# Optimization experiments

Measured on AMD Instinct MI355X. Metric: run time of the kernel, lower is better.

## Reference

```python
import jax, jax.numpy as jnp
import numpy as np

N = 50000       # nodes
E = 800000      # edges (before self-loops)
IN_DIM = 128
HID = 64
HEADS = 4
C = HID // HEADS  # 16 per-head channels
NEG_SLOPE = 0.2   # PyG GATConv default
BN_EPS = 1e-5


def setup_inputs() -> dict:
    key = jax.random.key(0)
    ks = jax.random.split(key, 16)
    inp = {
        "x": jax.random.normal(ks[0], (N, IN_DIM), jnp.float32),
        "edge_index": jax.random.randint(ks[1], (2, E), 0, N, dtype=jnp.int32),
    }
    def glorot(k, shape):
        fan = sum(shape)
        return jax.random.normal(k, shape, jnp.float32) * jnp.sqrt(2.0 / fan)
    # layer 0: in=IN_DIM, layer 1: in=HID
    inp["W0"] = glorot(ks[2], (IN_DIM, HEADS * C))
    inp["a_src0"] = glorot(ks[3], (HEADS, C))
    inp["a_dst0"] = glorot(ks[4], (HEADS, C))
    inp["b0"] = jnp.zeros((HEADS * C,), jnp.float32)
    inp["g0"] = jnp.ones((HID,), jnp.float32)
    inp["be0"] = jnp.zeros((HID,), jnp.float32)
    inp["W1"] = glorot(ks[5], (HID, HEADS * C))
    inp["a_src1"] = glorot(ks[6], (HEADS, C))
    inp["a_dst1"] = glorot(ks[7], (HEADS, C))
    inp["b1"] = jnp.zeros((HEADS * C,), jnp.float32)
    inp["g1"] = jnp.ones((HID,), jnp.float32)
    inp["be1"] = jnp.zeros((HID,), jnp.float32)
    return inp


def _segment_softmax(e, dst, n):
    # softmax over edges grouped by destination node, per head. e: [Et, H]
    m = jax.ops.segment_max(e, dst, num_segments=n)          # [N, H]
    ex = jnp.exp(e - m[dst])
    s = jax.ops.segment_sum(ex, dst, num_segments=n)         # [N, H]
    return ex / (s[dst] + 1e-16)


def _gat_conv(h, src, dst, W, a_s, a_d, b):
    n = h.shape[0]
    hp = (h @ W).reshape(n, HEADS, C)                        # [N, H, C]
    al_s = jnp.einsum('nhc,hc->nh', hp, a_s)                 # [N, H]
    al_d = jnp.einsum('nhc,hc->nh', hp, a_d)
    e = jax.nn.leaky_relu(al_s[src] + al_d[dst], NEG_SLOPE)  # [Et, H]
    alpha = _segment_softmax(e, dst, n)
    msg = hp[src] * alpha[:, :, None]                        # [Et, H, C]
    out = jax.ops.segment_sum(msg, dst, num_segments=n)      # [N, H, C]
    return out.reshape(n, HEADS * C) + b


def _batch_norm(h, g, b):
    mu = h.mean(axis=0)
    var = h.var(axis=0)
    return (h - mu) * jax.lax.rsqrt(var + BN_EPS) * g + b


def reference(x, edge_index, W0, a_src0, a_dst0, b0, g0, be0,
              W1, a_src1, a_dst1, b1, g1, be1):
    n = x.shape[0]
    loops = jnp.arange(n, dtype=edge_index.dtype)
    src = jnp.concatenate([edge_index[0], loops])  # PyG adds self-loops
    dst = jnp.concatenate([edge_index[1], loops])
    h = _gat_conv(x, src, dst, W0, a_src0, a_dst0, b0)
    h = _batch_norm(h, g0, be0)
    h = jax.nn.relu(h)  # dropout: identity (eval / deterministic)
    h = _gat_conv(h, src, dst, W1, a_src1, a_dst1, b1)
    h = _batch_norm(h, g1, be1)
    return h
```

## Files before the change

kernel.cpp:

```cpp
#include <hip/hip_runtime.h>
#include <hip/hip_fp16.h>

#define CAP 128

__device__ __forceinline__ float sel4(float4 v, int h) {
  return h == 0 ? v.x : h == 1 ? v.y : h == 2 ? v.z : v.w;
}

template<int K, bool APPLY_BN>
__global__ void __launch_bounds__(256, 4)
gemm_tiled(const float* __restrict__ X, const float* __restrict__ W,
           const float* __restrict__ a_s, const float* __restrict__ a_d,
           const float* __restrict__ bnsum, const float* __restrict__ bnsq,
           const float* __restrict__ g, const float* __restrict__ be,
           __half* __restrict__ hp, float* __restrict__ al_s,
           float* __restrict__ al_d, int n)
{
  __shared__ float Wl[(K / 4) * 64 * 4];
  __shared__ float Xt[64 * K];

  for (int gi = threadIdx.x; gi < (K / 4) * 64; gi += 256) {
    int k4 = gi >> 6, ln = gi & 63;
    float4 w;
    w.x = W[(k4 * 4 + 0) * 64 + ln];
    w.y = W[(k4 * 4 + 1) * 64 + ln];
    w.z = W[(k4 * 4 + 2) * 64 + ln];
    w.w = W[(k4 * 4 + 3) * 64 + ln];
    *(float4*)&Wl[gi * 4] = w;
  }

  int row0 = blockIdx.x * 64;
  int nrows = min(64, n - row0);
  float4 sc, sh;
  if (APPLY_BN) {
    int cg = (threadIdx.x & 15) * 4;
    float inv_n = 1.f / (float)n;
#pragma unroll
    for (int q = 0; q < 4; ++q) {
      float mu  = bnsum[cg + q] * inv_n;
      float var = bnsq[cg + q] * inv_n - mu * mu;
      float s   = g[cg + q] * rsqrtf(var + 1e-5f);
      ((float*)&sc)[q] = s;
      ((float*)&sh)[q] = be[cg + q] - mu * s;
    }
  }
  const float4* src = (const float4*)(X + (size_t)row0 * K);
  int nf4 = nrows * (K / 4);
  for (int i = threadIdx.x; i < nf4; i += 256) {
    float4 v = src[i];
    if (APPLY_BN) {
      v.x = fmaxf(v.x * sc.x + sh.x, 0.f);
      v.y = fmaxf(v.y * sc.y + sh.y, 0.f);
      v.z = fmaxf(v.z * sc.z + sh.z, 0.f);
      v.w = fmaxf(v.w * sc.w + sh.w, 0.f);
    }
    *(float4*)&Xt[i * 4] = v;
  }
  __syncthreads();

  int lane = threadIdx.x & 63;
  int wid  = threadIdx.x >> 6;
  int rbase = wid * 16;
  float acc[16];
#pragma unroll
  for (int r = 0; r < 16; ++r) acc[r] = 0.f;

  for (int k4 = 0; k4 < K / 4; ++k4) {
    float4 wv = *(const float4*)&Wl[(k4 * 64 + lane) * 4];
#pragma unroll
    for (int r = 0; r < 16; ++r) {
      float4 xv = *(const float4*)&Xt[(rbase + r) * K + k4 * 4];
      acc[r] += xv.x * wv.x + xv.y * wv.y + xv.z * wv.z + xv.w * wv.w;
    }
  }

  float as_l = a_s[lane], ad_l = a_d[lane];
  int h = lane >> 4, c = lane & 15;
#pragma unroll
  for (int r = 0; r < 16; ++r) {
    int lr = rbase + r;
    if (lr >= nrows) break;
    int row = row0 + lr;
    float a = acc[r];
    hp[(size_t)row * 64 + lane] = __float2half(a);
    float vs = a * as_l;
    float vd = a * ad_l;
#pragma unroll
    for (int off = 8; off >= 1; off >>= 1) {
      vs += __shfl_xor(vs, off, 64);
      vd += __shfl_xor(vd, off, 64);
    }
    if (c == 0) { al_s[row * 4 + h] = vs; al_d[row * 4 + h] = vd; }
  }
}

__global__ void hist_k(const int* __restrict__ ei, int E, int N, int* __restrict__ count)
{
  int e = blockIdx.x * 256 + threadIdx.x;
  int Et = E + N;
  if (e >= Et) return;
  int d = (e < E) ? ei[E + e] : (e - E);
  atomicAdd(&count[d], 1);
}

__global__ void scan_block_k(const int* __restrict__ count, int* __restrict__ row_ptr,
                             int* __restrict__ partial, int n)
{
  __shared__ int woff[16];
  int tid = threadIdx.x;
  int i = blockIdx.x * 1024 + tid;
  int v = (i < n) ? count[i] : 0;
  int lane = tid & 63, wid = tid >> 6;
  int incl = v;
#pragma unroll
  for (int off = 1; off < 64; off <<= 1) {
    int t = __shfl_up(incl, off, 64);
    if (lane >= off) incl += t;
  }
  if (lane == 63) woff[wid] = incl;
  __syncthreads();
  if (tid < 16) {
    int wv = woff[tid];
    int winc = wv;
#pragma unroll
    for (int off = 1; off < 16; off <<= 1) {
      int t = __shfl_up(winc, off, 64);
      if (tid >= off) winc += t;
    }
    woff[tid] = winc - wv;
    if (tid == 15) partial[blockIdx.x] = winc;
  }
  __syncthreads();
  if (i < n) row_ptr[i] = woff[wid] + incl - v;
}

__global__ void scan_partial_k(int* __restrict__ partial, int* __restrict__ row_ptr,
                               int nb, int n)
{
  int tid = threadIdx.x;
  int v = (tid < nb) ? partial[tid] : 0;
  int incl = v;
#pragma unroll
  for (int off = 1; off < 64; off <<= 1) {
    int t = __shfl_up(incl, off, 64);
    if (tid >= off) incl += t;
  }
  if (tid < nb) partial[tid] = incl - v;
  if (tid == 63) row_ptr[n] = incl;
}

__global__ void scan_add_k(int* __restrict__ row_ptr, int* __restrict__ cursor,
                           const int* __restrict__ partial, int n)
{
  int i = blockIdx.x * 1024 + threadIdx.x;
  if (i < n) {
    int r = row_ptr[i] + partial[blockIdx.x];
    row_ptr[i] = r;
    cursor[i] = r;
  }
}

__global__ void scatter_k(const int* __restrict__ ei, int E, int N,
                          int* __restrict__ cursor, int* __restrict__ col_src,
                          int* __restrict__ col_dst)
{
  int e = blockIdx.x * 256 + threadIdx.x;
  int Et = E + N;
  if (e >= Et) return;
  int s, d;
  if (e < E) { s = ei[e]; d = ei[E + e]; } else { s = d = e - E; }
  int pos = atomicAdd(&cursor[d], 1);
  col_src[pos] = s;
  col_dst[pos] = d;
}

__global__ void eweight_k(const int* __restrict__ csrc, const int* __restrict__ cdst,
                          const float* __restrict__ al_s, const float* __restrict__ al_d,
                          float4* __restrict__ ew, int Et)
{
  int e = blockIdx.x * 256 + threadIdx.x;
  if (e >= Et) return;
  int s = csrc[e], d = cdst[e];
  float4 a = *(const float4*)(al_s + (size_t)s * 4);
  float4 b = *(const float4*)(al_d + (size_t)d * 4);
  float ex = a.x + b.x; ex = ex >= 0.f ? ex : 0.2f * ex;
  float ey = a.y + b.y; ey = ey >= 0.f ? ey : 0.2f * ey;
  float ez = a.z + b.z; ez = ez >= 0.f ? ez : 0.2f * ez;
  float ewv = a.w + b.w; ewv = ewv >= 0.f ? ewv : 0.2f * ewv;
  ew[e] = make_float4(__expf(ex), __expf(ey), __expf(ez), __expf(ewv));
}

__global__ void __launch_bounds__(256)
node_agg(const int* __restrict__ row_ptr, const int* __restrict__ col_src,
         const float4* __restrict__ ew, const __half* __restrict__ hp,
         const float* __restrict__ bias, float* __restrict__ hpre,
         float* __restrict__ bnsum, float* __restrict__ bnsq, int n)
{
  __shared__ int   sh_s[4][CAP];
  __shared__ float sh_w[4][CAP * 4];
  __shared__ float shs[64], shq[64];

  int lane = threadIdx.x & 63;
  int wid  = threadIdx.x >> 6;
  int h    = lane >> 4;
  float b  = bias[lane];
  float lsum = 0.f, lsq = 0.f;
  int nwaves = gridDim.x * 4;
  int npairs = (n + 1) >> 1;

  for (int p = blockIdx.x * 4 + wid; p < npairs; p += nwaves) {
    int d = p * 2;
    bool has1 = (d + 1) < n;
    int beg0 = row_ptr[d];
    int end0 = row_ptr[d + 1];
    int end1 = has1 ? row_ptr[d + 2] : end0;
    int deg0 = end0 - beg0;
    int degP = end1 - beg0;
    float o0, o1 = 0.f;

    if (degP <= CAP) {
      float p00 = 0.f, p01 = 0.f, p02 = 0.f, p03 = 0.f;
      float p10 = 0.f, p11 = 0.f, p12 = 0.f, p13 = 0.f;
      for (int jb = 0; jb < degP; jb += 64) {
        int jj = jb + lane;
        if (jj < degP) {
          int s = col_src[beg0 + jj];
          float4 w = ew[beg0 + jj];
          sh_s[wid][jj] = s;
          *(float4*)&sh_w[wid][jj * 4] = w;
          if (jj < deg0) { p00 += w.x; p01 += w.y; p02 += w.z; p03 += w.w; }
          else           { p10 += w.x; p11 += w.y; p12 += w.z; p13 += w.w; }
        }
      }
#pragma unroll
      for (int off = 32; off >= 1; off >>= 1) {
        p00 += __shfl_xor(p00, off, 64); p01 += __shfl_xor(p01, off, 64);
        p02 += __shfl_xor(p02, off, 64); p03 += __shfl_xor(p03, off, 64);
        p10 += __shfl_xor(p10, off, 64); p11 += __shfl_xor(p11, off, 64);
        p12 += __shfl_xor(p12, off, 64); p13 += __shfl_xor(p13, off, 64);
      }
      float den0 = (h == 0) ? p00 : (h == 1) ? p01 : (h == 2) ? p02 : p03;
      float den1 = (h == 0) ? p10 : (h == 1) ? p11 : (h == 2) ? p12 : p13;

      float acc0 = 0.f, acc1 = 0.f;
      int j = 0;
      for (; j + 8 <= degP; j += 8) {
#pragma unroll
        for (int k = 0; k < 8; ++k) {
          int jk = j + k;
          int s = sh_s[wid][jk];
          float wh = sh_w[wid][jk * 4 + h];
          float v = __half2float(hp[(size_t)s * 64 + lane]);
          float w0 = (jk < deg0) ? wh : 0.f;
          acc0 += w0 * v;
          acc1 += (wh - w0) * v;
        }
      }
      for (; j < degP; ++j) {
        int s = sh_s[wid][j];
        float wh = sh_w[wid][j * 4 + h];
        float v = __half2float(hp[(size_t)s * 64 + lane]);
        float w0 = (j < deg0) ? wh : 0.f;
        acc0 += w0 * v;
        acc1 += (wh - w0) * v;
      }
      o0 = acc0 / (den0 + 1e-16f) + b;
      if (has1) o1 = acc1 / (den1 + 1e-16f) + b;
    } else {
      float den = 0.f, acc = 0.f;
      for (int j = beg0; j < end0; ++j) {
        float wh = sel4(ew[j], h);
        den += wh;
        acc += wh * __half2float(hp[(size_t)col_src[j] * 64 + lane]);
      }
      o0 = acc / (den + 1e-16f) + b;
      if (has1) {
        den = 0.f; acc = 0.f;
        for (int j = end0; j < end1; ++j) {
          float wh = sel4(ew[j], h);
          den += wh;
          acc += wh * __half2float(hp[(size_t)col_src[j] * 64 + lane]);
        }
        o1 = acc / (den + 1e-16f) + b;
      }
    }

    hpre[(size_t)d * 64 + lane] = o0;
    lsum += o0; lsq += o0 * o0;
    if (has1) {
      hpre[(size_t)(d + 1) * 64 + lane] = o1;
      lsum += o1; lsq += o1 * o1;
    }
  }

  if (threadIdx.x < 64) { shs[threadIdx.x] = 0.f; shq[threadIdx.x] = 0.f; }
  __syncthreads();
  atomicAdd(&shs[lane], lsum);
  atomicAdd(&shq[lane], lsq);
  __syncthreads();
  if (threadIdx.x < 64) {
    atomicAdd(&bnsum[threadIdx.x], shs[threadIdx.x]);
    atomicAdd(&bnsq[threadIdx.x],  shq[threadIdx.x]);
  }
}

__global__ void bn_apply(float* __restrict__ buf, const float* __restrict__ bnsum,
                         const float* __restrict__ bnsq, const float* __restrict__ g,
                         const float* __restrict__ be, int n)
{
  size_t i = (size_t)blockIdx.x * 256 + threadIdx.x;
  size_t total = (size_t)n * 64;
  if (i >= total) return;
  int c = (int)(i & 63);
  float inv_n = 1.f / (float)n;
  float mu  = bnsum[c] * inv_n;
  float var = bnsq[c] * inv_n - mu * mu;
  buf[i] = (buf[i] - mu) * rsqrtf(var + 1e-5f) * g[c] + be[c];
}

extern "C" void kernel_launch(void* const* d_in, const int* in_sizes, int n_in,
                              void* d_out, int out_size, void* d_ws, size_t ws_size,
                              hipStream_t stream) {
  const float* x   = (const float*)d_in[0];
  const int*   ei  = (const int*)d_in[1];
  const float* W0  = (const float*)d_in[2];
  const float* as0 = (const float*)d_in[3];
  const float* ad0 = (const float*)d_in[4];
  const float* b0  = (const float*)d_in[5];
  const float* g0  = (const float*)d_in[6];
  const float* be0 = (const float*)d_in[7];
  const float* W1  = (const float*)d_in[8];
  const float* as1 = (const float*)d_in[9];
  const float* ad1 = (const float*)d_in[10];
  const float* b1  = (const float*)d_in[11];
  const float* g1  = (const float*)d_in[12];
  const float* be1 = (const float*)d_in[13];
  float* out = (float*)d_out;

  int N = in_sizes[0] / 128;
  int E = in_sizes[1] / 2;
  int Et = E + N;

  char* w = (char*)d_ws;
  auto alloc = [&](size_t bytes) {
    char* p = w; w += (bytes + 255) & ~255ull; return p;
  };
  int*    count = (int*)alloc((size_t)N * 4 + 4 * 64 * 4);
  float*  bnsum0 = (float*)(count + N);
  float*  bnsq0  = bnsum0 + 64;
  float*  bnsum1 = bnsq0 + 64;
  float*  bnsq1  = bnsum1 + 64;
  __half* hp    = (__half*)alloc((size_t)N * 64 * 2);
  float*  hpre0 = (float*)alloc((size_t)N * 64 * 4);
  float*  als   = (float*)alloc((size_t)N * 4 * 4);
  float*  ald   = (float*)alloc((size_t)N * 4 * 4);
  int*    rowp  = (int*)alloc((size_t)(N + 1) * 4);
  int*    cursor= (int*)alloc((size_t)N * 4);
  int*    parts = (int*)alloc(64 * 4);
  int*    csrc  = (int*)alloc((size_t)Et * 4);
  int*    cdst  = (int*)alloc((size_t)Et * 4);
  float4* ew    = (float4*)alloc((size_t)Et * 16);

  dim3 blk(256);
  int gEt   = (Et + 255) / 256;
  int gN64  = (N * 64 + 255) / 256;
  int nb    = (N + 1023) / 1024;
  int gTile = (N + 63) / 64;

  hipMemsetAsync(count, 0, (size_t)N * 4 + 4 * 64 * 4, stream);

  hist_k<<<gEt, blk, 0, stream>>>(ei, E, N, count);
  scan_block_k<<<nb, 1024, 0, stream>>>(count, rowp, parts, N);
  scan_partial_k<<<1, 64, 0, stream>>>(parts, rowp, nb, N);
  scan_add_k<<<nb, 1024, 0, stream>>>(rowp, cursor, parts, N);
  scatter_k<<<gEt, blk, 0, stream>>>(ei, E, N, cursor, csrc, cdst);

  gemm_tiled<128, false><<<gTile, blk, 0, stream>>>(x, W0, as0, ad0,
                                                    nullptr, nullptr, nullptr, nullptr,
                                                    hp, als, ald, N);
  eweight_k<<<gEt, blk, 0, stream>>>(csrc, cdst, als, ald, ew, Et);
  node_agg<<<2048, blk, 0, stream>>>(rowp, csrc, ew, hp, b0,
                                     hpre0, bnsum0, bnsq0, N);

  gemm_tiled<64, true><<<gTile, blk, 0, stream>>>(hpre0, W1, as1, ad1,
                                                  bnsum0, bnsq0, g0, be0,
                                                  hp, als, ald, N);
  eweight_k<<<gEt, blk, 0, stream>>>(csrc, cdst, als, ald, ew, Et);
  node_agg<<<2048, blk, 0, stream>>>(rowp, csrc, ew, hp, b1,
                                     out, bnsum1, bnsq1, N);
  bn_apply<<<gN64, blk, 0, stream>>>(out, bnsum1, bnsq1, g1, be1, N);
}
```

Measured before the change: 331.4 us.

## Gather neighbor rows with 16-byte loads, one node per wave in aggregation

The aggregation kernel now handles one destination node per wave instead of two. Each group of 8 lanes reads a whole neighbor's 64 half-precision features with 16-byte vector loads, so 8 edges are processed at once. Partial sums are reduced across groups with cross-lane shuffles and transposed through shared memory. The grid is doubled to keep enough waves in flight. This is meant to cut the number of global load instructions and increase memory-level parallelism in the gather, at the cost of extra shuffle reductions per node and padding low-degree nodes up to a multiple of 8.

After: 421.1 us. +27.1%, slower.

```diff
diff --git a/kernel.cpp b/kernel.cpp
--- a/kernel.cpp
+++ b/kernel.cpp
@@ -5,6 +5,15 @@
 
 __device__ __forceinline__ float sel4(float4 v, int h) {
   return h == 0 ? v.x : h == 1 ? v.y : h == 2 ? v.z : v.w;
+}
+__device__ __forceinline__ float sel8(const float a[8], int k) {
+  float m0 = (k & 1) ? a[1] : a[0];
+  float m1 = (k & 1) ? a[3] : a[2];
+  float m2 = (k & 1) ? a[5] : a[4];
+  float m3 = (k & 1) ? a[7] : a[6];
+  float n0 = (k & 2) ? m1 : m0;
+  float n1 = (k & 2) ? m3 : m2;
+  return (k & 4) ? n1 : n0;
 }
 
 template<int K, bool APPLY_BN>
@@ -198,99 +207,90 @@
 {
   __shared__ int   sh_s[4][CAP];
   __shared__ float sh_w[4][CAP * 4];
+  __shared__ float sh_o[4][64];
   __shared__ float shs[64], shq[64];
 
   int lane = threadIdx.x & 63;
   int wid  = threadIdx.x >> 6;
-  int h    = lane >> 4;
+  int grp  = lane >> 3;
+  int q    = lane & 7;
+  int hq   = q >> 1;
   float b  = bias[lane];
   float lsum = 0.f, lsq = 0.f;
   int nwaves = gridDim.x * 4;
-  int npairs = (n + 1) >> 1;
-
-  for (int p = blockIdx.x * 4 + wid; p < npairs; p += nwaves) {
-    int d = p * 2;
-    bool has1 = (d + 1) < n;
-    int beg0 = row_ptr[d];
-    int end0 = row_ptr[d + 1];
-    int end1 = has1 ? row_ptr[d + 2] : end0;
-    int deg0 = end0 - beg0;
-    int degP = end1 - beg0;
-    float o0, o1 = 0.f;
-
-    if (degP <= CAP) {
-      float p00 = 0.f, p01 = 0.f, p02 = 0.f, p03 = 0.f;
-      float p10 = 0.f, p11 = 0.f, p12 = 0.f, p13 = 0.f;
-      for (int jb = 0; jb < degP; jb += 64) {
+
+  for (int d = blockIdx.x * 4 + wid; d < n; d += nwaves) {
+    int beg = row_ptr[d], end = row_ptr[d + 1];
+    int deg = end - beg;
+    float outv;
+
+    if (deg <= CAP) {
+      int degR = (deg + 7) & ~7;
+      float p0 = 0.f, p1 = 0.f, p2 = 0.f, p3 = 0.f;
+      for (int jb = 0; jb < degR; jb += 64) {
         int jj = jb + lane;
-        if (jj < degP) {
-          int s = col_src[beg0 + jj];
-          float4 w = ew[beg0 + jj];
+        int s = 0;
+        float4 w = make_float4(0.f, 0.f, 0.f, 0.f);
+        if (jj < deg) {
+          s = col_src[beg + jj];
+          w = ew[beg + jj];
+        }
+        if (jj < degR) {
           sh_s[wid][jj] = s;
           *(float4*)&sh_w[wid][jj * 4] = w;
-          if (jj < deg0) { p00 += w.x; p01 += w.y; p02 += w.z; p03 += w.w; }
-          else           { p10 += w.x; p11 += w.y; p12 += w.z; p13 += w.w; }
         }
+        p0 += w.x; p1 += w.y; p2 += w.z; p3 += w.w;
       }
 #pragma unroll
       for (int off = 32; off >= 1; off >>= 1) {
-        p00 += __shfl_xor(p00, off, 64); p01 += __shfl_xor(p01, off, 64);
-        p02 += __shfl_xor(p02, off, 64); p03 += __shfl_xor(p03, off, 64);
-        p10 += __shfl_xor(p10, off, 64); p11 += __shfl_xor(p11, off, 64);
-        p12 += __shfl_xor(p12, off, 64); p13 += __shfl_xor(p13, off, 64);
-      }
-      float den0 = (h == 0) ? p00 : (h == 1) ? p01 : (h == 2) ? p02 : p03;
-      float den1 = (h == 0) ? p10 : (h == 1) ? p11 : (h == 2) ? p12 : p13;
-
-      float acc0 = 0.f, acc1 = 0.f;
-      int j = 0;
-      for (; j + 8 <= degP; j += 8) {
-#pragma unroll
-        for (int k = 0; k < 8; ++k) {
-          int jk = j + k;
-          int s = sh_s[wid][jk];
-          float wh = sh_w[wid][jk * 4 + h];
-          float v = __half2float(hp[(size_t)s * 64 + lane]);
-          float w0 = (jk < deg0) ? wh : 0.f;
-          acc0 += w0 * v;
-          acc1 += (wh - w0) * v;
-        }
-      }
-      for (; j < degP; ++j) {
-        int s = sh_s[wid][j];
-        float wh = sh_w[wid][j * 4 + h];
-        float v = __half2float(hp[(size_t)s * 64 + lane]);
-        float w0 = (j < deg0) ? wh : 0.f;
-        acc0 += w0 * v;
-        acc1 += (wh - w0) * v;
-      }
-      o0 = acc0 / (den0 + 1e-16f) + b;
-      if (has1) o1 = acc1 / (den1 + 1e-16f) + b;
+        p0 += __shfl_xor(p0, off, 64);
+        p1 += __shfl_xor(p1, off, 64);
+        p2 += __shfl_xor(p2, off, 64);
+        p3 += __shfl_xor(p3, off, 64);
+      }
+
+      float acc[8];
+#pragma unroll
+      for (int k = 0; k < 8; ++k) acc[k] = 0.f;
+
+      for (int j = 0; j < degR; j += 8) {
+        int e = j + grp;
+        int s = sh_s[wid][e];
+        float wh = sh_w[wid][e * 4 + hq];
+        uint4 raw = *(const uint4*)(hp + (size_t)s * 64 + q * 8);
+        const __half2* hh = (const __half2*)&raw;
+        float2 f0 = __half22float2(hh[0]);
+        float2 f1 = __half22float2(hh[1]);
+        float2 f2 = __half22float2(hh[2]);
+        float2 f3 = __half22float2(hh[3]);
+        acc[0] += wh * f0.x; acc[1] += wh * f0.y;
+        acc[2] += wh * f1.x; acc[3] += wh * f1.y;
+        acc[4] += wh * f2.x; acc[5] += wh * f2.y;
+        acc[6] += wh * f3.x; acc[7] += wh * f3.y;
+      }
+#pragma unroll
+      for (int off = 8; off <= 32; off <<= 1) {
+#pragma unroll
+        for (int k = 0; k < 8; ++k) acc[k] += __shfl_xor(acc[k], off, 64);
+      }
+      float v = sel8(acc, grp);
+      sh_o[wid][q * 8 + grp] = v;
+      __builtin_amdgcn_wave_barrier();
+      float den = (lane < 16) ? p0 : (lane < 32) ? p1 : (lane < 48) ? p2 : p3;
+      outv = sh_o[wid][lane] / (den + 1e-16f) + b;
     } else {
+      int h = lane >> 4;
       float den = 0.f, acc = 0.f;
-      for (int j = beg0; j < end0; ++j) {
+      for (int j = beg; j < end; ++j) {
         float wh = sel4(ew[j], h);
         den += wh;
         acc += wh * __half2float(hp[(size_t)col_src[j] * 64 + lane]);
       }
-      o0 = acc / (den + 1e-16f) + b;
-      if (has1) {
-        den = 0.f; acc = 0.f;
-        for (int j = end0; j < end1; ++j) {
-          float wh = sel4(ew[j], h);
-          den += wh;
-          acc += wh * __half2float(hp[(size_t)col_src[j] * 64 + lane]);
-        }
-        o1 = acc / (den + 1e-16f) + b;
-      }
-    }
-
-    hpre[(size_t)d * 64 + lane] = o0;
-    lsum += o0; lsq += o0 * o0;
-    if (has1) {
-      hpre[(size_t)(d + 1) * 64 + lane] = o1;
-      lsum += o1; lsq += o1 * o1;
-    }
+      outv = acc / (den + 1e-16f) + b;
+    }
+
+    hpre[(size_t)d * 64 + lane] = outv;
+    lsum += outv; lsq += outv * outv;
   }
 
   if (threadIdx.x < 64) { shs[threadIdx.x] = 0.f; shq[threadIdx.x] = 0.f; }
@@ -379,14 +379,14 @@
                                                     nullptr, nullptr, nullptr, nullptr,
                                                     hp, als, ald, N);
   eweight_k<<<gEt, blk, 0, stream>>>(csrc, cdst, als, ald, ew, Et);
-  node_agg<<<2048, blk, 0, stream>>>(rowp, csrc, ew, hp, b0,
+  node_agg<<<4096, blk, 0, stream>>>(rowp, csrc, ew, hp, b0,
                                      hpre0, bnsum0, bnsq0, N);
 
   gemm_tiled<64, true><<<gTile, blk, 0, stream>>>(hpre0, W1, as1, ad1,
                                                   bnsum0, bnsq0, g0, be0,
                                                   hp, als, ald, N);
   eweight_k<<<gEt, blk, 0, stream>>>(csrc, cdst, als, ald, ew, Et);
-  node_agg<<<2048, blk, 0, stream>>>(rowp, csrc, ew, hp, b1,
+  node_agg<<<4096, blk, 0, stream>>>(rowp, csrc, ew, hp, b1,
                                      out, bnsum1, bnsq1, N);
   bn_apply<<<gN64, blk, 0, stream>>>(out, bnsum1, bnsq1, g1, be1, N);
 }
```
